# Optimization experiments

Hardware: AMD Instinct MI355X
Metric: run time of the kernel (lower is better)

## Reference

```python
import jax, jax.numpy as jnp
import numpy as np

EPS = 1e-9
LDIM = 4  # dim_g + dim_t + dim_b + dim_w


def _mvn_logpdf(v, F):
    # batched zero-mean multivariate normal log-density, v: (N,O), F: (N,O,O)
    chol = jnp.linalg.cholesky(F)
    z = jax.scipy.linalg.solve_triangular(chol, v[..., None], lower=True)[..., 0]
    quad = jnp.sum(z * z, axis=-1)
    logdet = 2.0 * jnp.sum(jnp.log(jnp.diagonal(chol, axis1=-2, axis2=-1)), axis=-1)
    k = v.shape[-1]
    return -0.5 * (quad + logdet + k * jnp.log(2.0 * jnp.pi))


def _forward(y, B_G, B_T, B_B, B_W, lambda_r1_free, lambda_r2_free,
             q_diag, r_diag, gamma1, gamma2_learnable):
    N, Nt, O = y.shape
    L = LDIM
    # ----- _build_matrices -----
    B11 = jnp.zeros((L, L)).at[0, 0].set(B_G[0, 0]).at[1, 1].set(B_T[0, 0]).at[2, 2].set(B_B[0, 0])
    B22 = jnp.zeros((L, L)).at[3, 3].set(B_W[0, 0])
    B12 = jnp.zeros((L, L)).at[3, :3].set(1.0 / 3.0)  # regime1 factors feed shared factor
    B21 = jnp.zeros((L, L))
    L1 = jnp.zeros((O, L))
    L1 = L1.at[0, 0].set(1.0).at[1, 0].set(lambda_r1_free[0]).at[2, 0].set(lambda_r1_free[1])
    L1 = L1.at[3, 1].set(1.0).at[4, 1].set(lambda_r1_free[2]).at[5, 1].set(lambda_r1_free[3])
    L1 = L1.at[6, 2].set(1.0).at[7, 2].set(lambda_r1_free[4]).at[8, 2].set(lambda_r1_free[5])
    L2 = jnp.zeros((O, L)).at[0, 3].set(1.0).at[1:, 3].set(lambda_r2_free)
    Q = jnp.diag(jnp.abs(q_diag) + 1e-4)
    R = jnp.diag(jnp.abs(r_diag) + 1e-4)
    F_JIT = 1e-5 * jnp.eye(O)
    I_L = jnp.eye(L)
    P22_CONST = 0.9999

    # ----- initial beliefs ('informative') -----
    prob0 = jnp.tile(jnp.array([0.99, 0.01], jnp.float32), (N, 1))
    eta0 = jnp.zeros((N, L), y.dtype)
    P0 = jnp.tile(jnp.diag(jnp.array([1000.0, 1000.0, 1000.0, 1e-9], y.dtype))[None], (N, 1, 1))

    def predict(B, eta, P):
        # eta: (N,L), P: (N,L,L)
        return eta @ B.T, jnp.einsum('ij,njk,lk->nil', B, P, B) + Q

    def innov(Lm, e, Pp, y_t):
        v = y_t - e @ Lm.T
        F = jnp.einsum('oi,nij,pj->nop', Lm, Pp, Lm) + R + F_JIT
        return v, F

    def kupdate(e, Pp, Lm, v, F):
        LP = jnp.einsum('oi,nij->noj', Lm, Pp)          # (N,O,L)
        K = jnp.swapaxes(jnp.linalg.solve(F, LP), -1, -2)  # P Lm^T F^{-1}, (N,L,O)
        e_u = e + jnp.einsum('nlo,no->nl', K, v)
        IKL = I_L - K @ Lm                                # (N,L,L)
        P_u = IKL @ Pp @ jnp.swapaxes(IKL, -1, -2) + jnp.einsum('nlo,op,nmp->nlm', K, R, K)
        return e_u, P_u

    def collapse(w_a, w_b, e_a, e_b, P_a, P_b):
        e = w_a[:, None] * e_a + w_b[:, None] * e_b
        da, db = e_a - e, e_b - e
        P = (w_a[:, None, None] * (P_a + da[:, :, None] * da[:, None, :])
             + w_b[:, None, None] * (P_b + db[:, :, None] * db[:, None, :]))
        return e, P

    def step(carry, y_t):
        prob, eta1, eta2, P1, P2, ll = carry
        # HMM transition: p11 depends on regime-1 state (first L-1 components)
        logit_p11 = gamma1 + eta1[:, :3] @ gamma2_learnable
        p11 = jax.nn.sigmoid(logit_p11)
        # predictions for the 4 regime transitions (origin -> destination)
        e11, Pp11 = predict(B11, eta1, P1)
        e12, Pp12 = predict(B21, eta2, P2)
        e21, Pp21 = predict(B12, eta1, P1)
        e22, Pp22 = predict(B22, eta2, P2)
        v11, F11 = innov(L1, e11, Pp11, y_t)
        v12, F12 = innov(L1, e12, Pp12, y_t)
        v21, F21 = innov(L2, e21, Pp21, y_t)
        v22, F22 = innov(L2, e22, Pp22, y_t)
        ll11 = _mvn_logpdf(v11, F11)
        ll12 = _mvn_logpdf(v12, F12)
        ll21 = _mvn_logpdf(v21, F21)
        ll22 = _mvn_logpdf(v22, F22)
        lp = jnp.log(prob + EPS)
        c11 = lp[:, 0] + jnp.log(p11 + EPS) + ll11
        c12 = lp[:, 1] + np.log(1.0 - P22_CONST + EPS) + ll12
        c21 = lp[:, 0] + jnp.log(1.0 - p11 + EPS) + ll21
        c22 = lp[:, 1] + np.log(P22_CONST + EPS) + ll22
        logp = jnp.stack([c11, c12, c21, c22], axis=1)
        ll_t = jax.scipy.special.logsumexp(logp, axis=1)
        pt = jnp.exp(logp - ll_t[:, None])
        pr1 = pt[:, 0] + pt[:, 1]
        pr2 = pt[:, 2] + pt[:, 3]
        W11 = pt[:, 0] / (pr1 + EPS)
        W12 = pt[:, 1] / (pr1 + EPS)
        W21 = pt[:, 2] / (pr2 + EPS)
        W22 = pt[:, 3] / (pr2 + EPS)
        eu11, Pu11 = kupdate(e11, Pp11, L1, v11, F11)
        eu12, Pu12 = kupdate(e12, Pp12, L1, v12, F12)
        eu21, Pu21 = kupdate(e21, Pp21, L2, v21, F21)
        eu22, Pu22 = kupdate(e22, Pp22, L2, v22, F22)
        eta1n, P1n = collapse(W11, W12, eu11, eu12, Pu11, Pu12)
        eta2n, P2n = collapse(W21, W22, eu21, eu22, Pu21, Pu22)
        probn = jnp.stack([pr1, pr2], axis=1)
        return (probn, eta1n, eta2n, P1n, P2n, ll + ll_t.sum()), None

    carry0 = (prob0, eta0, eta0, P0, P0, jnp.zeros((), y.dtype))
    (_, _, _, _, _, total_ll), _ = jax.lax.scan(step, carry0, jnp.swapaxes(y, 0, 1))
    return total_ll


def setup_inputs() -> dict:
    key = jax.random.key(0)
    ks = jax.random.split(key, 12)
    N, Nt, O = 16384, 64, 9
    f32 = jnp.float32
    return {
        'y': jax.random.normal(ks[0], (N, Nt, O), f32),
        'B_G': jax.random.uniform(ks[1], (1, 1), f32, 0.6, 0.95),  # Beta(5,1.5)-like AR coeffs
        'B_T': jax.random.uniform(ks[2], (1, 1), f32, 0.6, 0.95),
        'B_B': jax.random.uniform(ks[3], (1, 1), f32, 0.6, 0.95),
        'B_W': jax.random.uniform(ks[4], (1, 1), f32, 0.6, 0.95),
        'lambda_r1_free': jax.random.normal(ks[5], (6,), f32),
        'lambda_r2_free': jax.random.normal(ks[6], (O - 1,), f32),
        'q_diag': jax.random.uniform(ks[7], (LDIM,), f32),
        'r_diag': jax.random.uniform(ks[8], (O,), f32),
        'gamma1': jnp.abs(jax.random.normal(ks[9], (), f32)),
        'gamma2_learnable': jax.random.normal(ks[10], (LDIM - 1,), f32),
    }


def reference(y, B_G, B_T, B_B, B_W, lambda_r1_free, lambda_r2_free,
              q_diag, r_diag, gamma1, gamma2_learnable):
    return _forward(y, B_G, B_T, B_B, B_W, lambda_r1_free, lambda_r2_free,
                    q_diag, r_diag, gamma1, gamma2_learnable)
```

## Files before the change

kernel.cpp:

```cpp
#include <hip/hip_runtime.h>


typedef float v2f __attribute__((ext_vector_type(2)));

static __device__ __forceinline__ float frcp(float x)  { return __builtin_amdgcn_rcpf(x); }
static __device__ __forceinline__ float frsq(float x)  { return __builtin_amdgcn_rsqf(x); }
static __device__ __forceinline__ float fexp2(float x) { return __builtin_amdgcn_exp2f(x); }
static __device__ __forceinline__ float flog2(float x) { return __builtin_amdgcn_logf(x); }

template <int CTRL>
static __device__ __forceinline__ float dppf(float x) {
    int i = __float_as_int(x);
    i = __builtin_amdgcn_mov_dpp(i, CTRL, 0xF, 0xF, true);
    return __int_as_float(i);
}
#define ROTL 0xC9
#define ROTR 0xD2
#define XOR1 0xB1
#define XOR2 0x4E

static __device__ __forceinline__ float qsum(float x) {
    x += dppf<XOR1>(x);
    x += dppf<XOR2>(x);
    return x;
}

#define EPSF   1e-9f
#define L2E    1.4426950408889634f
#define LN2    0.6931471805599453f
#define L2_2PI_9 23.86346461225016f
#define C12F   1.00001e-4f
#define P22F   0.99990001f
#define QK     (-0.5f * L2E)

__global__ __launch_bounds__(64, 1)
void kf_kernel(const float* __restrict__ y,
               const float* __restrict__ pBG, const float* __restrict__ pBT,
               const float* __restrict__ pBB, const float* __restrict__ pBW,
               const float* __restrict__ lam1, const float* __restrict__ lam2,
               const float* __restrict__ qd,  const float* __restrict__ rd,
               const float* __restrict__ pG1, const float* __restrict__ pG2,
               float* __restrict__ partial, int N, int Nt)
{
    const int lane = threadIdx.x;
    const int j    = lane & 3;
    const int sid  = (blockIdx.x * 64 + lane) >> 2;
    const bool valid = (sid < N);
    const bool isRow = (j < 3);
    const int jj = isRow ? j : 0;
    const int rowlen = Nt * 9;
    const int nchunk = Nt / 4;

    const float bg = pBG[0], bt = pBT[0], bb = pBB[0], bw = pBW[0];
    float a[9], l2v[9], id[9], ld[9];
    a[0] = 1.f; a[1] = lam1[0]; a[2] = lam1[1];
    a[3] = 1.f; a[4] = lam1[2]; a[5] = lam1[3];
    a[6] = 1.f; a[7] = lam1[4]; a[8] = lam1[5];
    l2v[0] = 1.f;
    #pragma unroll
    for (int i = 0; i < 8; ++i) l2v[i + 1] = lam2[i];
    float l2detD = 0.f;
    #pragma unroll
    for (int o = 0; o < 9; ++o) {
        float dv = fabsf(rd[o]) + 1.0e-4f + 1.0e-5f;
        id[o] = 1.0f / dv;
        ld[o] = l2v[o] * id[o];
        l2detD += flog2(dv);
    }
    const float q0 = fabsf(qd[0]) + 1e-4f, q1 = fabsf(qd[1]) + 1e-4f;
    const float q2 = fabsf(qd[2]) + 1e-4f, q3 = fabsf(qd[3]) + 1e-4f;
    const float g0 = a[0]*a[0]*id[0] + a[1]*a[1]*id[1] + a[2]*a[2]*id[2];
    const float g1 = a[3]*a[3]*id[3] + a[4]*a[4]*id[4] + a[5]*a[5]*id[5];
    const float g2 = a[6]*a[6]*id[6] + a[7]*a[7]*id[7] + a[8]*a[8]*id[8];
    float h = 0.f;
    #pragma unroll
    for (int o = 0; o < 9; ++o) h += l2v[o] * ld[o];
    const float pk0 = q0 / (1.f + q0 * g0);
    const float pk1 = q1 / (1.f + q1 * g1);
    const float pk2 = q2 / (1.f + q2 * g2);
    const float C12D = C12F * frsq((1.f + q0*g0) * (1.f + q1*g1) * (1.f + q2*g2));
    const float gam1 = pG1[0], w0c = pG2[0], w1c = pG2[1], w2c = pG2[2];
    const float CC = -0.5f * (l2detD + L2_2PI_9);

    auto sel3 = [&](float x0, float x1, float x2) {
        float r = (jj == 1) ? x1 : x0;
        return (jj == 2) ? x2 : r;
    };
    const float aO0 = sel3(a[0], a[3], a[6]), aO1 = sel3(a[1], a[4], a[7]), aO2 = sel3(a[2], a[5], a[8]);
    const float iO0 = sel3(id[0], id[3], id[6]), iO1 = sel3(id[1], id[4], id[7]), iO2 = sel3(id[2], id[5], id[8]);
    const float lO0 = sel3(ld[0], ld[3], ld[6]), lO1 = sel3(ld[1], ld[4], ld[7]), lO2 = sel3(ld[2], ld[5], ld[8]);
    const float bS = sel3(bg, bt, bb), bN = sel3(bt, bb, bg), bP = sel3(bb, bg, bt);
    const float gS = sel3(g0, g1, g2), gN = sel3(g1, g2, g0), gP = sel3(g2, g0, g1);
    const float qS = sel3(q0, q1, q2);
    const float pkS = sel3(pk0, pk1, pk2);
    const float wS = sel3(w0c, w1c, w2c);

    auto z3 = [&](float x) { return isRow ? x : 0.0f; };

    float pf1 = 0.99f + EPSF, pf2 = 0.01f + EPSF;
    float seJ = 0.f;
    float Pr0 = 1000.f, Pr1 = 0.f, Pr2 = 0.f;
    float sm2 = 0.f, sp2 = 1e-9f;
    float acc2 = 0.0f;

    const float* row = y + (size_t)(valid ? sid : 0) * rowlen + 3 * jj;
    float A[12], B[12];
    auto loadChunk = [&](float (&buf)[12], int c) {
        const float* p = row + c * 36;
        #pragma unroll
        for (int s = 0; s < 4; ++s) {
            buf[s*3+0] = p[s*9+0];
            buf[s*3+1] = p[s*9+1];
            buf[s*3+2] = p[s*9+2];
        }
    };
    loadChunk(A, 0);

    auto step4 = [&](const float (&buf)[12]) {
        #pragma unroll
        for (int s = 0; s < 4; ++s) {
            const float y0 = buf[s*3+0], y1 = buf[s*3+1], y2 = buf[s*3+2];

            float logit = gam1 + qsum(z3(wS * seJ));
            float esig = fexp2(-logit * L2E);
            float p11 = frcp(1.f + esig);
            float pf11 = p11 + EPSF, pf21 = 1.f - p11 + EPSF;

            float epJ = bS * seJ;
            float S0 = bS*bS*Pr0 + qS;
            float S1 = bS*bN*Pr1;
            float S2 = bS*bP*Pr2;
            float M0 = S0*gS + 1.f;
            float M1 = S1*gN;
            float M2 = S2*gP;

            float v0 = y0 - aO0*epJ, v1 = y1 - aO1*epJ, v2 = y2 - aO2*epJ;
            float w0v = iO0*v0, w1v = iO1*v1, w2v = iO2*v2;
            float uJ = aO0*w0v + aO1*w1v + aO2*w2v;
            float vdv = qsum(z3(v0*w0v + v1*w1v + v2*w2v));
            float yl  = qsum(z3(lO0*y0 + lO1*y1 + lO2*y2));
            float ydy = vdv + qsum(z3(epJ * (2.f*uJ + gS*epJ)));

            float Mn0 = dppf<ROTL>(M0), Mn1 = dppf<ROTL>(M1), Mn2 = dppf<ROTL>(M2);
            float Mp0 = dppf<ROTR>(M0), Mp1 = dppf<ROTR>(M1), Mp2 = dppf<ROTR>(M2);
            float cf0 = Mn0*Mp0 - Mn1*Mp2;
            float cf1 = Mn1*Mp1 - Mn2*Mp0;
            float cf2 = Mn2*Mp2 - Mn0*Mp1;
            float det = M0*cf0 + M1*cf1 + M2*cf2;
            float rs  = frsq(det);
            float iM  = rs * rs;
            float cn0 = dppf<ROTL>(cf0), cn1 = dppf<ROTL>(cf1), cn2 = dppf<ROTL>(cf2);
            float cp0 = dppf<ROTR>(cf0), cp1 = dppf<ROTR>(cf1), cp2 = dppf<ROTR>(cf2);
            float Ci0 = iM * (S0*cf0 + S1*cn2 + S2*cp1);
            float Ci1 = iM * (S0*cf1 + S1*cn0 + S2*cp2);
            float Ci2 = iM * (S0*cf2 + S1*cn1 + S2*cp0);

            float uN = dppf<ROTL>(uJ), uP = dppf<ROTR>(uJ);
            float tJ = Ci0*uJ + Ci1*uN + Ci2*uP;
            float quad11 = vdv - qsum(z3(uJ * tJ));
            float euJ = epJ + tJ;

            float u12 = uJ + gS * epJ;
            float fJ  = pkS * u12;
            float quad12 = ydy - qsum(z3(pkS * u12 * u12));

            float seS = qsum(z3(seJ));
            float sP  = qsum(z3(Pr0 + Pr1 + Pr2));
            v2f m2v; m2v.x = seS * (1.f/3.f);       m2v.y = bw * sm2;
            v2f pvv; pvv.x = q3 + sP * (1.f/9.f);   pvv.y = bw*bw*sp2 + q3;
            v2f u1v  = (v2f){yl, yl} - m2v * (v2f){h, h};
            v2f vdav = (v2f){ydy, ydy} - m2v * ((v2f){2.f*yl, 2.f*yl} - m2v * (v2f){h, h});
            v2f denv = (v2f){1.f, 1.f} + pvv * (v2f){h, h};
            v2f rvv; rvv.x = frsq(denv.x); rvv.y = frsq(denv.y);
            v2f idev = rvv * rvv;
            v2f puv = pvv * idev;
            v2f quadv = vdav - puv * u1v * u1v;
            v2f euv = m2v + puv * u1v;

            float q11e = QK * quad11, q12e = QK * quad12;
            float q21e = QK * quadv.x, q22e = QK * quadv.y;
            float Mq = fmaxf(fmaxf(q11e, q12e), fmaxf(q21e, q22e));
            float w11 = pf1 * pf11 * rs    * fexp2(q11e - Mq);
            float w12 = pf2 * C12D         * fexp2(q12e - Mq);
            float w21 = pf1 * pf21 * rvv.x * fexp2(q21e - Mq);
            float w22 = pf2 * P22F * rvv.y * fexp2(q22e - Mq);
            float ssum = w11 + w12 + w21 + w22;
            acc2 += Mq + flog2(ssum);
            float pr1n = w11 + w12, pr2n = w21 + w22;
            float den1 = pr1n + EPSF * ssum, den2 = pr2n + EPSF * ssum;
            float inv1 = frcp(den1), inv2 = frcp(den2), issum = frcp(ssum);
            float W11 = w11*inv1, W12 = w12*inv1;
            float W21 = w21*inv2, W22 = w22*inv2;
            pf1 = pr1n * issum + EPSF;
            pf2 = pr2n * issum + EPSF;

            float neJ = W11*euJ + W12*fJ;
            float daJ = euJ - neJ, dbJ = fJ - neJ;
            float daN = dppf<ROTL>(daJ), daP = dppf<ROTR>(daJ);
            float dbN = dppf<ROTL>(dbJ), dbP = dppf<ROTR>(dbJ);
            Pr0 = W11*(Ci0 + daJ*daJ) + W12*(pkS + dbJ*dbJ);
            Pr1 = W11*(Ci1 + daJ*daN) + W12*(dbJ*dbN);
            Pr2 = W11*(Ci2 + daJ*daP) + W12*(dbJ*dbP);
            seJ = neJ;

            float nm2 = W21*euv.x + W22*euv.y;
            float dc = euv.x - nm2, dd = euv.y - nm2;
            sp2 = W21*(puv.x + dc*dc) + W22*(puv.y + dd*dd);
            sm2 = nm2;
        }
    };

    for (int c = 0; c < nchunk; c += 2) {
        if (c + 1 < nchunk) loadChunk(B, c + 1);
        step4(A);
        if (c + 2 < nchunk) loadChunk(A, c + 2);
        step4(B);
    }

    float acc = (valid && j == 0) ? (acc2 + (float)Nt * CC) * LN2 : 0.0f;
    #pragma unroll
    for (int off = 32; off; off >>= 1) acc += __shfl_down(acc, off, 64);
    if (lane == 0) partial[blockIdx.x] = acc;
}

__global__ __launch_bounds__(64)
void reduce_k(const float* __restrict__ part, float* __restrict__ out, int nb)
{
    float s = 0.f;
    for (int i = threadIdx.x; i < nb; i += 64) s += part[i];
    #pragma unroll
    for (int off = 32; off; off >>= 1) s += __shfl_down(s, off, 64);
    if (threadIdx.x == 0) out[0] = s;
}

extern "C" void kernel_launch(void* const* d_in, const int* in_sizes, int n_in,
                              void* d_out, int out_size, void* d_ws, size_t ws_size,
                              hipStream_t stream)
{
    const float* y    = (const float*)d_in[0];
    const float* pBG  = (const float*)d_in[1];
    const float* pBT  = (const float*)d_in[2];
    const float* pBB  = (const float*)d_in[3];
    const float* pBW  = (const float*)d_in[4];
    const float* lam1 = (const float*)d_in[5];
    const float* lam2 = (const float*)d_in[6];
    const float* qd   = (const float*)d_in[7];
    const float* rd   = (const float*)d_in[8];
    const float* pG1  = (const float*)d_in[9];
    const float* pG2  = (const float*)d_in[10];

    const int total = in_sizes[0];
    const int Nt = 64, O = 9;
    const int N = total / (Nt * O);
    const int blocks = (N * 4 + 63) / 64;

    float* partial = (float*)d_ws;
    kf_kernel<<<blocks, 64, 0, stream>>>(y, pBG, pBT, pBB, pBW, lam1, lam2,
                                         qd, rd, pG1, pG2, partial, N, Nt);
    reduce_k<<<1, 64, 0, stream>>>(partial, (float*)d_out, blocks);
}
```

Measured before the change: 123.8 us.

## Process two sequences per 4-lane group using packed float2 math

Each 4-lane group now filters two independent sequences at once, holding state in float2 vectors so the compiler can emit packed FP32 instructions and gain instruction-level parallelism across the serial recurrence. The launch uses half as many blocks. Row masking moves from per-use selects into constants premultiplied by a row mask. This costs roughly twice the registers per thread and halves the number of waves, which reduces latency hiding through occupancy.

Result: slower. 133.1 us (+7.5%).

```diff
diff --git a/kernel.cpp b/kernel.cpp
--- a/kernel.cpp
+++ b/kernel.cpp
@@ -19,11 +19,21 @@
 #define XOR1 0xB1
 #define XOR2 0x4E
 
-static __device__ __forceinline__ float qsum(float x) {
-    x += dppf<XOR1>(x);
-    x += dppf<XOR2>(x);
+template <int CTRL>
+static __device__ __forceinline__ v2f dpp2(v2f v) {
+    v2f r; r.x = dppf<CTRL>(v.x); r.y = dppf<CTRL>(v.y); return r;
+}
+static __device__ __forceinline__ v2f qsum2(v2f x) {
+    x += dpp2<XOR1>(x);
+    x += dpp2<XOR2>(x);
     return x;
 }
+static __device__ __forceinline__ v2f sp(float x) { return (v2f){x, x}; }
+static __device__ __forceinline__ v2f rcp2(v2f a)  { return (v2f){frcp(a.x),  frcp(a.y)};  }
+static __device__ __forceinline__ v2f rsq2(v2f a)  { return (v2f){frsq(a.x),  frsq(a.y)};  }
+static __device__ __forceinline__ v2f exp22(v2f a) { return (v2f){fexp2(a.x), fexp2(a.y)}; }
+static __device__ __forceinline__ v2f log22(v2f a) { return (v2f){flog2(a.x), flog2(a.y)}; }
+static __device__ __forceinline__ v2f max2(v2f a, v2f b) { return (v2f){fmaxf(a.x,b.x), fmaxf(a.y,b.y)}; }
 
 #define EPSF   1e-9f
 #define L2E    1.4426950408889634f
@@ -44,10 +54,12 @@
 {
     const int lane = threadIdx.x;
     const int j    = lane & 3;
-    const int sid  = (blockIdx.x * 64 + lane) >> 2;
-    const bool valid = (sid < N);
+    const int qi   = (blockIdx.x * 64 + lane) >> 2;
+    const int sidA = 2 * qi, sidB = 2 * qi + 1;
+    const bool vA = (sidA < N), vB = (sidB < N);
     const bool isRow = (j < 3);
     const int jj = isRow ? j : 0;
+    const float mrow = isRow ? 1.f : 0.f;
     const int rowlen = Nt * 9;
     const int nchunk = Nt / 4;
 
@@ -87,125 +99,141 @@
         return (jj == 2) ? x2 : r;
     };
     const float aO0 = sel3(a[0], a[3], a[6]), aO1 = sel3(a[1], a[4], a[7]), aO2 = sel3(a[2], a[5], a[8]);
-    const float iO0 = sel3(id[0], id[3], id[6]), iO1 = sel3(id[1], id[4], id[7]), iO2 = sel3(id[2], id[5], id[8]);
-    const float lO0 = sel3(ld[0], ld[3], ld[6]), lO1 = sel3(ld[1], ld[4], ld[7]), lO2 = sel3(ld[2], ld[5], ld[8]);
-    const float bS = sel3(bg, bt, bb), bN = sel3(bt, bb, bg), bP = sel3(bb, bg, bt);
+    const float iO0 = sel3(id[0], id[3], id[6]) * mrow, iO1 = sel3(id[1], id[4], id[7]) * mrow,
+                iO2 = sel3(id[2], id[5], id[8]) * mrow;
+    const float lO0 = sel3(ld[0], ld[3], ld[6]) * mrow, lO1 = sel3(ld[1], ld[4], ld[7]) * mrow,
+                lO2 = sel3(ld[2], ld[5], ld[8]) * mrow;
+    const float bS = sel3(bg, bt, bb) * mrow;
+    const float bS2 = bS * bS;
+    const float bSN = bS * sel3(bt, bb, bg);
+    const float bSP = bS * sel3(bb, bg, bt);
     const float gS = sel3(g0, g1, g2), gN = sel3(g1, g2, g0), gP = sel3(g2, g0, g1);
-    const float qS = sel3(q0, q1, q2);
-    const float pkS = sel3(pk0, pk1, pk2);
-    const float wS = sel3(w0c, w1c, w2c);
-
-    auto z3 = [&](float x) { return isRow ? x : 0.0f; };
-
-    float pf1 = 0.99f + EPSF, pf2 = 0.01f + EPSF;
-    float seJ = 0.f;
-    float Pr0 = 1000.f, Pr1 = 0.f, Pr2 = 0.f;
-    float sm2 = 0.f, sp2 = 1e-9f;
-    float acc2 = 0.0f;
-
-    const float* row = y + (size_t)(valid ? sid : 0) * rowlen + 3 * jj;
-    float A[12], B[12];
-    auto loadChunk = [&](float (&buf)[12], int c) {
-        const float* p = row + c * 36;
+    const float qS  = sel3(q0, q1, q2) * mrow;
+    const float pkS = sel3(pk0, pk1, pk2) * mrow;
+    const float wS  = sel3(w0c, w1c, w2c) * mrow;
+
+    v2f pf1 = sp(0.99f + EPSF), pf2 = sp(0.01f + EPSF);
+    v2f seJ = sp(0.f);
+    v2f Pr0 = sp(isRow ? 1000.f : 0.f), Pr1 = sp(0.f), Pr2 = sp(0.f);
+    v2f sm2 = sp(0.f), sp2 = sp(1e-9f);
+    v2f acc2 = sp(0.f);
+
+    const float* rowA = y + (size_t)(vA ? sidA : 0) * rowlen + 3 * jj;
+    const float* rowB = y + (size_t)(vB ? sidB : 0) * rowlen + 3 * jj;
+    v2f A[12], B[12];
+    auto loadChunk = [&](v2f (&buf)[12], int c) {
+        const float* pA = rowA + c * 36;
+        const float* pB = rowB + c * 36;
         #pragma unroll
         for (int s = 0; s < 4; ++s) {
-            buf[s*3+0] = p[s*9+0];
-            buf[s*3+1] = p[s*9+1];
-            buf[s*3+2] = p[s*9+2];
+            #pragma unroll
+            for (int k = 0; k < 3; ++k) {
+                buf[s*3+k].x = pA[s*9+k];
+                buf[s*3+k].y = pB[s*9+k];
+            }
         }
     };
     loadChunk(A, 0);
 
-    auto step4 = [&](const float (&buf)[12]) {
+    auto step4 = [&](const v2f (&buf)[12]) {
         #pragma unroll
         for (int s = 0; s < 4; ++s) {
-            const float y0 = buf[s*3+0], y1 = buf[s*3+1], y2 = buf[s*3+2];
-
-            float logit = gam1 + qsum(z3(wS * seJ));
-            float esig = fexp2(-logit * L2E);
-            float p11 = frcp(1.f + esig);
-            float pf11 = p11 + EPSF, pf21 = 1.f - p11 + EPSF;
-
-            float epJ = bS * seJ;
-            float S0 = bS*bS*Pr0 + qS;
-            float S1 = bS*bN*Pr1;
-            float S2 = bS*bP*Pr2;
-            float M0 = S0*gS + 1.f;
-            float M1 = S1*gN;
-            float M2 = S2*gP;
-
-            float v0 = y0 - aO0*epJ, v1 = y1 - aO1*epJ, v2 = y2 - aO2*epJ;
-            float w0v = iO0*v0, w1v = iO1*v1, w2v = iO2*v2;
-            float uJ = aO0*w0v + aO1*w1v + aO2*w2v;
-            float vdv = qsum(z3(v0*w0v + v1*w1v + v2*w2v));
-            float yl  = qsum(z3(lO0*y0 + lO1*y1 + lO2*y2));
-            float ydy = vdv + qsum(z3(epJ * (2.f*uJ + gS*epJ)));
-
-            float Mn0 = dppf<ROTL>(M0), Mn1 = dppf<ROTL>(M1), Mn2 = dppf<ROTL>(M2);
-            float Mp0 = dppf<ROTR>(M0), Mp1 = dppf<ROTR>(M1), Mp2 = dppf<ROTR>(M2);
-            float cf0 = Mn0*Mp0 - Mn1*Mp2;
-            float cf1 = Mn1*Mp1 - Mn2*Mp0;
-            float cf2 = Mn2*Mp2 - Mn0*Mp1;
-            float det = M0*cf0 + M1*cf1 + M2*cf2;
-            float rs  = frsq(det);
-            float iM  = rs * rs;
-            float cn0 = dppf<ROTL>(cf0), cn1 = dppf<ROTL>(cf1), cn2 = dppf<ROTL>(cf2);
-            float cp0 = dppf<ROTR>(cf0), cp1 = dppf<ROTR>(cf1), cp2 = dppf<ROTR>(cf2);
-            float Ci0 = iM * (S0*cf0 + S1*cn2 + S2*cp1);
-            float Ci1 = iM * (S0*cf1 + S1*cn0 + S2*cp2);
-            float Ci2 = iM * (S0*cf2 + S1*cn1 + S2*cp0);
-
-            float uN = dppf<ROTL>(uJ), uP = dppf<ROTR>(uJ);
-            float tJ = Ci0*uJ + Ci1*uN + Ci2*uP;
-            float quad11 = vdv - qsum(z3(uJ * tJ));
-            float euJ = epJ + tJ;
-
-            float u12 = uJ + gS * epJ;
-            float fJ  = pkS * u12;
-            float quad12 = ydy - qsum(z3(pkS * u12 * u12));
-
-            float seS = qsum(z3(seJ));
-            float sP  = qsum(z3(Pr0 + Pr1 + Pr2));
-            v2f m2v; m2v.x = seS * (1.f/3.f);       m2v.y = bw * sm2;
-            v2f pvv; pvv.x = q3 + sP * (1.f/9.f);   pvv.y = bw*bw*sp2 + q3;
-            v2f u1v  = (v2f){yl, yl} - m2v * (v2f){h, h};
-            v2f vdav = (v2f){ydy, ydy} - m2v * ((v2f){2.f*yl, 2.f*yl} - m2v * (v2f){h, h});
-            v2f denv = (v2f){1.f, 1.f} + pvv * (v2f){h, h};
-            v2f rvv; rvv.x = frsq(denv.x); rvv.y = frsq(denv.y);
-            v2f idev = rvv * rvv;
-            v2f puv = pvv * idev;
-            v2f quadv = vdav - puv * u1v * u1v;
-            v2f euv = m2v + puv * u1v;
-
-            float q11e = QK * quad11, q12e = QK * quad12;
-            float q21e = QK * quadv.x, q22e = QK * quadv.y;
-            float Mq = fmaxf(fmaxf(q11e, q12e), fmaxf(q21e, q22e));
-            float w11 = pf1 * pf11 * rs    * fexp2(q11e - Mq);
-            float w12 = pf2 * C12D         * fexp2(q12e - Mq);
-            float w21 = pf1 * pf21 * rvv.x * fexp2(q21e - Mq);
-            float w22 = pf2 * P22F * rvv.y * fexp2(q22e - Mq);
-            float ssum = w11 + w12 + w21 + w22;
-            acc2 += Mq + flog2(ssum);
-            float pr1n = w11 + w12, pr2n = w21 + w22;
-            float den1 = pr1n + EPSF * ssum, den2 = pr2n + EPSF * ssum;
-            float inv1 = frcp(den1), inv2 = frcp(den2), issum = frcp(ssum);
-            float W11 = w11*inv1, W12 = w12*inv1;
-            float W21 = w21*inv2, W22 = w22*inv2;
-            pf1 = pr1n * issum + EPSF;
-            pf2 = pr2n * issum + EPSF;
-
-            float neJ = W11*euJ + W12*fJ;
-            float daJ = euJ - neJ, dbJ = fJ - neJ;
-            float daN = dppf<ROTL>(daJ), daP = dppf<ROTR>(daJ);
-            float dbN = dppf<ROTL>(dbJ), dbP = dppf<ROTR>(dbJ);
-            Pr0 = W11*(Ci0 + daJ*daJ) + W12*(pkS + dbJ*dbJ);
+            const v2f y0 = buf[s*3+0], y1 = buf[s*3+1], y2 = buf[s*3+2];
+
+            v2f logit = sp(gam1) + qsum2(sp(wS) * seJ);
+            v2f esig = exp22(logit * sp(-L2E));
+            v2f p11 = rcp2(sp(1.f) + esig);
+            v2f pf11 = p11 + sp(EPSF);
+            v2f pf21 = sp(1.f) - p11 + sp(EPSF);
+
+            v2f epJ = sp(bS) * seJ;
+            v2f S0 = sp(bS2) * Pr0 + sp(qS);
+            v2f S1 = sp(bSN) * Pr1;
+            v2f S2 = sp(bSP) * Pr2;
+            v2f M0 = S0 * sp(gS) + sp(1.f);
+            v2f M1 = S1 * sp(gN);
+            v2f M2 = S2 * sp(gP);
+
+            v2f v0 = y0 - sp(aO0)*epJ;
+            v2f v1 = y1 - sp(aO1)*epJ;
+            v2f v2 = y2 - sp(aO2)*epJ;
+            v2f w0 = sp(iO0)*v0, w1 = sp(iO1)*v1, w2 = sp(iO2)*v2;
+            v2f uJ = sp(aO0)*w0 + sp(aO1)*w1 + sp(aO2)*w2;
+            v2f r1 = v0*w0 + v1*w1 + v2*w2;
+            v2f yl  = qsum2(sp(lO0)*y0 + sp(lO1)*y1 + sp(lO2)*y2);
+            v2f ydy = qsum2(r1 + epJ*(sp(2.f)*uJ + sp(gS)*epJ));
+
+            v2f Mn0 = dpp2<ROTL>(M0), Mn1 = dpp2<ROTL>(M1), Mn2 = dpp2<ROTL>(M2);
+            v2f Mp0 = dpp2<ROTR>(M0), Mp1 = dpp2<ROTR>(M1), Mp2 = dpp2<ROTR>(M2);
+            v2f cf0 = Mn0*Mp0 - Mn1*Mp2;
+            v2f cf1 = Mn1*Mp1 - Mn2*Mp0;
+            v2f cf2 = Mn2*Mp2 - Mn0*Mp1;
+            v2f det = M0*cf0 + M1*cf1 + M2*cf2;
+            v2f rs  = rsq2(det);
+            v2f iM  = rs * rs;
+            v2f cn0 = dpp2<ROTL>(cf0), cn1 = dpp2<ROTL>(cf1), cn2 = dpp2<ROTL>(cf2);
+            v2f cp0 = dpp2<ROTR>(cf0), cp1 = dpp2<ROTR>(cf1), cp2 = dpp2<ROTR>(cf2);
+            v2f Ci0 = iM * (S0*cf0 + S1*cn2 + S2*cp1);
+            v2f Ci1 = iM * (S0*cf1 + S1*cn0 + S2*cp2);
+            v2f Ci2 = iM * (S0*cf2 + S1*cn1 + S2*cp0);
+
+            v2f uN = dpp2<ROTL>(uJ), uP = dpp2<ROTR>(uJ);
+            v2f tJ = Ci0*uJ + Ci1*uN + Ci2*uP;
+            v2f quad11 = qsum2(r1 - uJ*tJ);
+            v2f euJ = epJ + tJ;
+
+            v2f u12 = uJ + sp(gS)*epJ;
+            v2f fJ  = sp(pkS) * u12;
+            v2f quad12 = ydy - qsum2(sp(pkS)*u12*u12);
+
+            v2f seS = qsum2(seJ);
+            v2f sP  = qsum2(Pr0 + Pr1 + Pr2);
+            v2f m2_1 = seS * sp(1.f/3.f);
+            v2f m2_2 = sp(bw) * sm2;
+            v2f pv_1 = sp(q3) + sP * sp(1.f/9.f);
+            v2f pv_2 = sp(bw*bw)*sp2 + sp(q3);
+            v2f u1_1 = yl - m2_1*sp(h);
+            v2f u1_2 = yl - m2_2*sp(h);
+            v2f vda_1 = ydy - m2_1*(sp(2.f)*yl - m2_1*sp(h));
+            v2f vda_2 = ydy - m2_2*(sp(2.f)*yl - m2_2*sp(h));
+            v2f den_1 = sp(1.f) + pv_1*sp(h);
+            v2f den_2 = sp(1.f) + pv_2*sp(h);
+            v2f rv_1 = rsq2(den_1), rv_2 = rsq2(den_2);
+            v2f pu_1 = pv_1*(rv_1*rv_1), pu_2 = pv_2*(rv_2*rv_2);
+            v2f quad21 = vda_1 - pu_1*u1_1*u1_1;
+            v2f quad22 = vda_2 - pu_2*u1_2*u1_2;
+            v2f eu_1 = m2_1 + pu_1*u1_1;
+            v2f eu_2 = m2_2 + pu_2*u1_2;
+
+            v2f q11e = sp(QK)*quad11, q12e = sp(QK)*quad12;
+            v2f q21e = sp(QK)*quad21, q22e = sp(QK)*quad22;
+            v2f Mq = max2(max2(q11e, q12e), max2(q21e, q22e));
+            v2f w11 = pf1*pf11*rs        * exp22(q11e - Mq);
+            v2f w12 = pf2*sp(C12D)       * exp22(q12e - Mq);
+            v2f w21 = pf1*pf21*rv_1      * exp22(q21e - Mq);
+            v2f w22 = pf2*sp(P22F)*rv_2  * exp22(q22e - Mq);
+            v2f ssum = w11 + w12 + w21 + w22;
+            acc2 += Mq + log22(ssum);
+            v2f pr1n = w11 + w12, pr2n = w21 + w22;
+            v2f den1 = pr1n + sp(EPSF)*ssum, den2 = pr2n + sp(EPSF)*ssum;
+            v2f inv1 = rcp2(den1), inv2 = rcp2(den2), issum = rcp2(ssum);
+            v2f W11 = w11*inv1, W12 = w12*inv1;
+            v2f W21 = w21*inv2, W22 = w22*inv2;
+            pf1 = pr1n*issum + sp(EPSF);
+            pf2 = pr2n*issum + sp(EPSF);
+
+            v2f neJ = W11*euJ + W12*fJ;
+            v2f daJ = euJ - neJ, dbJ = fJ - neJ;
+            v2f daN = dpp2<ROTL>(daJ), daP = dpp2<ROTR>(daJ);
+            v2f dbN = dpp2<ROTL>(dbJ), dbP = dpp2<ROTR>(dbJ);
+            Pr0 = W11*(Ci0 + daJ*daJ) + W12*(sp(pkS) + dbJ*dbJ);
             Pr1 = W11*(Ci1 + daJ*daN) + W12*(dbJ*dbN);
             Pr2 = W11*(Ci2 + daJ*daP) + W12*(dbJ*dbP);
             seJ = neJ;
 
-            float nm2 = W21*euv.x + W22*euv.y;
-            float dc = euv.x - nm2, dd = euv.y - nm2;
-            sp2 = W21*(puv.x + dc*dc) + W22*(puv.y + dd*dd);
+            v2f nm2 = W21*eu_1 + W22*eu_2;
+            v2f dc = eu_1 - nm2, dd = eu_2 - nm2;
+            sp2 = W21*(pu_1 + dc*dc) + W22*(pu_2 + dd*dd);
             sm2 = nm2;
         }
     };
@@ -217,7 +245,11 @@
         step4(B);
     }
 
-    float acc = (valid && j == 0) ? (acc2 + (float)Nt * CC) * LN2 : 0.0f;
+    float acc = 0.f;
+    if (j == 0) {
+        if (vA) acc += (acc2.x + (float)Nt * CC) * LN2;
+        if (vB) acc += (acc2.y + (float)Nt * CC) * LN2;
+    }
     #pragma unroll
     for (int off = 32; off; off >>= 1) acc += __shfl_down(acc, off, 64);
     if (lane == 0) partial[blockIdx.x] = acc;
@@ -252,7 +284,8 @@
     const int total = in_sizes[0];
     const int Nt = 64, O = 9;
     const int N = total / (Nt * O);
-    const int blocks = (N * 4 + 63) / 64;
+    const int nq = (N + 1) / 2;
+    const int blocks = (nq * 4 + 63) / 64;
 
     float* partial = (float*)d_ws;
     kf_kernel<<<blocks, 64, 0, stream>>>(y, pBG, pBT, pBB, pBW, lam1, lam2,
```

## Map one series per thread instead of four lanes with DPP exchanges

Applied to the files above, without the earlier changes.

Replaces the 4-lanes-per-series decomposition, which used DPP rotations and quad sums to share the 3x3 covariance across lanes, with one thread per series that holds the full symmetric 3x3 covariance and 9 observations in registers. This removes the cross-lane DPP traffic and the idle fourth lane, and cuts the grid to a quarter of the blocks. In exchange there is more serial arithmetic and register pressure per thread, and only 256 single-wave blocks, which may underfill the GPU's compute units and leave too few waves to hide latency.

Result: slower. 130.4 us (+5.4%).

```diff
diff --git a/kernel.cpp b/kernel.cpp
--- a/kernel.cpp
+++ b/kernel.cpp
@@ -1,29 +1,10 @@
 #include <hip/hip_runtime.h>
 
-
-typedef float v2f __attribute__((ext_vector_type(2)));
 
 static __device__ __forceinline__ float frcp(float x)  { return __builtin_amdgcn_rcpf(x); }
 static __device__ __forceinline__ float frsq(float x)  { return __builtin_amdgcn_rsqf(x); }
 static __device__ __forceinline__ float fexp2(float x) { return __builtin_amdgcn_exp2f(x); }
 static __device__ __forceinline__ float flog2(float x) { return __builtin_amdgcn_logf(x); }
-
-template <int CTRL>
-static __device__ __forceinline__ float dppf(float x) {
-    int i = __float_as_int(x);
-    i = __builtin_amdgcn_mov_dpp(i, CTRL, 0xF, 0xF, true);
-    return __int_as_float(i);
-}
-#define ROTL 0xC9
-#define ROTR 0xD2
-#define XOR1 0xB1
-#define XOR2 0x4E
-
-static __device__ __forceinline__ float qsum(float x) {
-    x += dppf<XOR1>(x);
-    x += dppf<XOR2>(x);
-    return x;
-}
 
 #define EPSF   1e-9f
 #define L2E    1.4426950408889634f
@@ -43,19 +24,15 @@
                float* __restrict__ partial, int N, int Nt)
 {
     const int lane = threadIdx.x;
-    const int j    = lane & 3;
-    const int sid  = (blockIdx.x * 64 + lane) >> 2;
+    const int sid  = blockIdx.x * 64 + lane;
     const bool valid = (sid < N);
-    const bool isRow = (j < 3);
-    const int jj = isRow ? j : 0;
     const int rowlen = Nt * 9;
-    const int nchunk = Nt / 4;
 
     const float bg = pBG[0], bt = pBT[0], bb = pBB[0], bw = pBW[0];
-    float a[9], l2v[9], id[9], ld[9];
-    a[0] = 1.f; a[1] = lam1[0]; a[2] = lam1[1];
-    a[3] = 1.f; a[4] = lam1[2]; a[5] = lam1[3];
-    a[6] = 1.f; a[7] = lam1[4]; a[8] = lam1[5];
+    const float a1 = lam1[0], a2 = lam1[1];
+    const float a4 = lam1[2], a5 = lam1[3];
+    const float a7 = lam1[4], a8 = lam1[5];
+    float l2v[9], id[9], ld[9];
     l2v[0] = 1.f;
     #pragma unroll
     for (int i = 0; i < 8; ++i) l2v[i + 1] = lam2[i];
@@ -67,11 +44,20 @@
         ld[o] = l2v[o] * id[o];
         l2detD += flog2(dv);
     }
+    const float id0 = id[0], id1 = id[1], id2 = id[2],
+                id3 = id[3], id4 = id[4], id5 = id[5],
+                id6 = id[6], id7 = id[7], id8 = id[8];
+    const float ld0 = ld[0], ld1 = ld[1], ld2 = ld[2],
+                ld3 = ld[3], ld4 = ld[4], ld5 = ld[5],
+                ld6 = ld[6], ld7 = ld[7], ld8 = ld[8];
+    const float aid0 = id0,      aid1 = a1 * id1, aid2 = a2 * id2;
+    const float aid3 = id3,      aid4 = a4 * id4, aid5 = a5 * id5;
+    const float aid6 = id6,      aid7 = a7 * id7, aid8 = a8 * id8;
     const float q0 = fabsf(qd[0]) + 1e-4f, q1 = fabsf(qd[1]) + 1e-4f;
     const float q2 = fabsf(qd[2]) + 1e-4f, q3 = fabsf(qd[3]) + 1e-4f;
-    const float g0 = a[0]*a[0]*id[0] + a[1]*a[1]*id[1] + a[2]*a[2]*id[2];
-    const float g1 = a[3]*a[3]*id[3] + a[4]*a[4]*id[4] + a[5]*a[5]*id[5];
-    const float g2 = a[6]*a[6]*id[6] + a[7]*a[7]*id[7] + a[8]*a[8]*id[8];
+    const float g0 = id0 + a1*a1*id1 + a2*a2*id2;
+    const float g1 = id3 + a4*a4*id4 + a5*a5*id5;
+    const float g2 = id6 + a7*a7*id7 + a8*a8*id8;
     float h = 0.f;
     #pragma unroll
     for (int o = 0; o < 9; ++o) h += l2v[o] * ld[o];
@@ -81,143 +67,144 @@
     const float C12D = C12F * frsq((1.f + q0*g0) * (1.f + q1*g1) * (1.f + q2*g2));
     const float gam1 = pG1[0], w0c = pG2[0], w1c = pG2[1], w2c = pG2[2];
     const float CC = -0.5f * (l2detD + L2_2PI_9);
-
-    auto sel3 = [&](float x0, float x1, float x2) {
-        float r = (jj == 1) ? x1 : x0;
-        return (jj == 2) ? x2 : r;
+    const float bg2 = bg*bg, bt2 = bt*bt, bb2 = bb*bb, bw2 = bw*bw;
+    const float bgbt = bg*bt, bgbb = bg*bb, btbb = bt*bb;
+
+    float pf1 = 0.99f + EPSF, pf2 = 0.01f + EPSF;
+    float se0 = 0.f, se1 = 0.f, se2 = 0.f;
+    float p00 = 1000.f, p01 = 0.f, p02 = 0.f, p11 = 1000.f, p12 = 0.f, p22 = 1000.f;
+    float sm2 = 0.f, sp2 = 1e-9f;
+    float acc2 = 0.f;
+
+    const float* row = y + (size_t)(valid ? sid : 0) * rowlen;
+    float A[9], B[9];
+    #pragma unroll
+    for (int k = 0; k < 9; ++k) A[k] = row[k];
+
+    auto step = [&](const float (&Y)[9]) {
+        float logit = gam1 + w0c*se0 + w1c*se1 + w2c*se2;
+        float p11s = frcp(1.f + fexp2(-logit * L2E));
+        float pf11 = p11s + EPSF, pf21 = 1.f - p11s + EPSF;
+
+        float e0 = bg*se0, e1 = bt*se1, e2 = bb*se2;
+        float s00 = bg2*p00 + q0, s11 = bt2*p11 + q1, s22 = bb2*p22 + q2;
+        float s01 = bgbt*p01, s02 = bgbb*p02, s12 = btbb*p12;
+
+        float v0 = Y[0] - e0,    v1 = Y[1] - a1*e0, v2 = Y[2] - a2*e0;
+        float v3 = Y[3] - e1,    v4 = Y[4] - a4*e1, v5 = Y[5] - a5*e1;
+        float v6 = Y[6] - e2,    v7 = Y[7] - a7*e2, v8 = Y[8] - a8*e2;
+        float u0 = aid0*v0 + aid1*v1 + aid2*v2;
+        float u1 = aid3*v3 + aid4*v4 + aid5*v5;
+        float u2 = aid6*v6 + aid7*v7 + aid8*v8;
+        float vdv = (id0*v0)*v0 + (id1*v1)*v1 + (id2*v2)*v2
+                  + (id3*v3)*v3 + (id4*v4)*v4 + (id5*v5)*v5
+                  + (id6*v6)*v6 + (id7*v7)*v7 + (id8*v8)*v8;
+        float yl  = ld0*Y[0] + ld1*Y[1] + ld2*Y[2]
+                  + ld3*Y[3] + ld4*Y[4] + ld5*Y[5]
+                  + ld6*Y[6] + ld7*Y[7] + ld8*Y[8];
+        float k0 = 2.f*u0 + g0*e0, k1 = 2.f*u1 + g1*e1, k2 = 2.f*u2 + g2*e2;
+        float ydy = vdv + e0*k0 + e1*k1 + e2*k2;
+
+        float m00 = s00*g0 + 1.f, m01 = s01*g1,       m02 = s02*g2;
+        float m10 = s01*g0,       m11 = s11*g1 + 1.f, m12 = s12*g2;
+        float m20 = s02*g0,       m21 = s12*g1,       m22 = s22*g2 + 1.f;
+        float c00 = m11*m22 - m12*m21;
+        float c01 = m12*m20 - m10*m22;
+        float c02 = m10*m21 - m11*m20;
+        float c10 = m02*m21 - m01*m22;
+        float c11 = m00*m22 - m02*m20;
+        float c12 = m01*m20 - m00*m21;
+        float c20 = m01*m12 - m02*m11;
+        float c21 = m02*m10 - m00*m12;
+        float c22 = m00*m11 - m01*m10;
+        float det = m00*c00 + m01*c01 + m02*c02;
+        float rs  = frsq(det);
+        float iM  = rs * rs;
+        float Ci00 = (s00*c00 + s01*c10 + s02*c20) * iM;
+        float Ci01 = (s00*c01 + s01*c11 + s02*c21) * iM;
+        float Ci02 = (s00*c02 + s01*c12 + s02*c22) * iM;
+        float Ci11 = (s01*c01 + s11*c11 + s12*c21) * iM;
+        float Ci12 = (s01*c02 + s11*c12 + s12*c22) * iM;
+        float Ci22 = (s02*c02 + s12*c12 + s22*c22) * iM;
+
+        float t0 = Ci00*u0 + Ci01*u1 + Ci02*u2;
+        float t1 = Ci01*u0 + Ci11*u1 + Ci12*u2;
+        float t2 = Ci02*u0 + Ci12*u1 + Ci22*u2;
+        float quad11 = vdv - (u0*t0 + u1*t1 + u2*t2);
+        float eu0 = e0 + t0, eu1 = e1 + t1, eu2 = e2 + t2;
+
+        float u120 = u0 + g0*e0, u121 = u1 + g1*e1, u122 = u2 + g2*e2;
+        float f0 = pk0*u120, f1 = pk1*u121, f2 = pk2*u122;
+        float quad12 = ydy - (f0*u120 + f1*u121 + f2*u122);
+
+        float seS = se0 + se1 + se2;
+        float sPs = p00 + p11 + p22 + 2.f*(p01 + p02 + p12);
+        float m2a = seS * (1.f/3.f);
+        float m2b = bw * sm2;
+        float pva = q3 + sPs * (1.f/9.f);
+        float pvb = bw2*sp2 + q3;
+        float u1a = yl - m2a*h;
+        float u1b = yl - m2b*h;
+        float vdaa = ydy - m2a*(2.f*yl - m2a*h);
+        float vdab = ydy - m2b*(2.f*yl - m2b*h);
+        float rva = frsq(1.f + pva*h);
+        float rvb = frsq(1.f + pvb*h);
+        float pua = pva*(rva*rva);
+        float pub = pvb*(rvb*rvb);
+        float quad21 = vdaa - pua*u1a*u1a;
+        float quad22 = vdab - pub*u1b*u1b;
+        float eua = m2a + pua*u1a;
+        float eub = m2b + pub*u1b;
+
+        float q11e = QK*quad11, q12e = QK*quad12;
+        float q21e = QK*quad21, q22e = QK*quad22;
+        float Mq = fmaxf(fmaxf(q11e, q12e), fmaxf(q21e, q22e));
+        float w11 = pf1*pf11*rs   * fexp2(q11e - Mq);
+        float w12 = pf2*C12D      * fexp2(q12e - Mq);
+        float w21 = pf1*pf21*rva  * fexp2(q21e - Mq);
+        float w22 = pf2*P22F*rvb  * fexp2(q22e - Mq);
+        float ssum = (w11 + w12) + (w21 + w22);
+        acc2 += Mq + flog2(ssum);
+        float pr1n = w11 + w12, pr2n = w21 + w22;
+        float inv1 = frcp(pr1n + EPSF*ssum);
+        float inv2 = frcp(pr2n + EPSF*ssum);
+        float issum = frcp(ssum);
+        float W11 = w11*inv1, W12 = w12*inv1;
+        float W21 = w21*inv2, W22 = w22*inv2;
+        pf1 = pr1n*issum + EPSF;
+        pf2 = pr2n*issum + EPSF;
+
+        float ne0 = W11*eu0 + W12*f0;
+        float ne1 = W11*eu1 + W12*f1;
+        float ne2 = W11*eu2 + W12*f2;
+        float da0 = eu0-ne0, da1 = eu1-ne1, da2 = eu2-ne2;
+        float db0 = f0-ne0,  db1 = f1-ne1,  db2 = f2-ne2;
+        p00 = W11*(Ci00 + da0*da0) + W12*(pk0 + db0*db0);
+        p01 = W11*(Ci01 + da0*da1) + W12*(db0*db1);
+        p02 = W11*(Ci02 + da0*da2) + W12*(db0*db2);
+        p11 = W11*(Ci11 + da1*da1) + W12*(pk1 + db1*db1);
+        p12 = W11*(Ci12 + da1*da2) + W12*(db1*db2);
+        p22 = W11*(Ci22 + da2*da2) + W12*(pk2 + db2*db2);
+        se0 = ne0; se1 = ne1; se2 = ne2;
+
+        float nm2 = W21*eua + W22*eub;
+        float dc = eua-nm2, dd = eub-nm2;
+        sp2 = W21*(pua + dc*dc) + W22*(pub + dd*dd);
+        sm2 = nm2;
     };
-    const float aO0 = sel3(a[0], a[3], a[6]), aO1 = sel3(a[1], a[4], a[7]), aO2 = sel3(a[2], a[5], a[8]);
-    const float iO0 = sel3(id[0], id[3], id[6]), iO1 = sel3(id[1], id[4], id[7]), iO2 = sel3(id[2], id[5], id[8]);
-    const float lO0 = sel3(ld[0], ld[3], ld[6]), lO1 = sel3(ld[1], ld[4], ld[7]), lO2 = sel3(ld[2], ld[5], ld[8]);
-    const float bS = sel3(bg, bt, bb), bN = sel3(bt, bb, bg), bP = sel3(bb, bg, bt);
-    const float gS = sel3(g0, g1, g2), gN = sel3(g1, g2, g0), gP = sel3(g2, g0, g1);
-    const float qS = sel3(q0, q1, q2);
-    const float pkS = sel3(pk0, pk1, pk2);
-    const float wS = sel3(w0c, w1c, w2c);
-
-    auto z3 = [&](float x) { return isRow ? x : 0.0f; };
-
-    float pf1 = 0.99f + EPSF, pf2 = 0.01f + EPSF;
-    float seJ = 0.f;
-    float Pr0 = 1000.f, Pr1 = 0.f, Pr2 = 0.f;
-    float sm2 = 0.f, sp2 = 1e-9f;
-    float acc2 = 0.0f;
-
-    const float* row = y + (size_t)(valid ? sid : 0) * rowlen + 3 * jj;
-    float A[12], B[12];
-    auto loadChunk = [&](float (&buf)[12], int c) {
-        const float* p = row + c * 36;
+
+    for (int t = 0; t < Nt; t += 2) {
         #pragma unroll
-        for (int s = 0; s < 4; ++s) {
-            buf[s*3+0] = p[s*9+0];
-            buf[s*3+1] = p[s*9+1];
-            buf[s*3+2] = p[s*9+2];
+        for (int k = 0; k < 9; ++k) B[k] = row[(t+1)*9 + k];
+        step(A);
+        if (t + 2 < Nt) {
+            #pragma unroll
+            for (int k = 0; k < 9; ++k) A[k] = row[(t+2)*9 + k];
         }
-    };
-    loadChunk(A, 0);
-
-    auto step4 = [&](const float (&buf)[12]) {
-        #pragma unroll
-        for (int s = 0; s < 4; ++s) {
-            const float y0 = buf[s*3+0], y1 = buf[s*3+1], y2 = buf[s*3+2];
-
-            float logit = gam1 + qsum(z3(wS * seJ));
-            float esig = fexp2(-logit * L2E);
-            float p11 = frcp(1.f + esig);
-            float pf11 = p11 + EPSF, pf21 = 1.f - p11 + EPSF;
-
-            float epJ = bS * seJ;
-            float S0 = bS*bS*Pr0 + qS;
-            float S1 = bS*bN*Pr1;
-            float S2 = bS*bP*Pr2;
-            float M0 = S0*gS + 1.f;
-            float M1 = S1*gN;
-            float M2 = S2*gP;
-
-            float v0 = y0 - aO0*epJ, v1 = y1 - aO1*epJ, v2 = y2 - aO2*epJ;
-            float w0v = iO0*v0, w1v = iO1*v1, w2v = iO2*v2;
-            float uJ = aO0*w0v + aO1*w1v + aO2*w2v;
-            float vdv = qsum(z3(v0*w0v + v1*w1v + v2*w2v));
-            float yl  = qsum(z3(lO0*y0 + lO1*y1 + lO2*y2));
-            float ydy = vdv + qsum(z3(epJ * (2.f*uJ + gS*epJ)));
-
-            float Mn0 = dppf<ROTL>(M0), Mn1 = dppf<ROTL>(M1), Mn2 = dppf<ROTL>(M2);
-            float Mp0 = dppf<ROTR>(M0), Mp1 = dppf<ROTR>(M1), Mp2 = dppf<ROTR>(M2);
-            float cf0 = Mn0*Mp0 - Mn1*Mp2;
-            float cf1 = Mn1*Mp1 - Mn2*Mp0;
-            float cf2 = Mn2*Mp2 - Mn0*Mp1;
-            float det = M0*cf0 + M1*cf1 + M2*cf2;
-            float rs  = frsq(det);
-            float iM  = rs * rs;
-            float cn0 = dppf<ROTL>(cf0), cn1 = dppf<ROTL>(cf1), cn2 = dppf<ROTL>(cf2);
-            float cp0 = dppf<ROTR>(cf0), cp1 = dppf<ROTR>(cf1), cp2 = dppf<ROTR>(cf2);
-            float Ci0 = iM * (S0*cf0 + S1*cn2 + S2*cp1);
-            float Ci1 = iM * (S0*cf1 + S1*cn0 + S2*cp2);
-            float Ci2 = iM * (S0*cf2 + S1*cn1 + S2*cp0);
-
-            float uN = dppf<ROTL>(uJ), uP = dppf<ROTR>(uJ);
-            float tJ = Ci0*uJ + Ci1*uN + Ci2*uP;
-            float quad11 = vdv - qsum(z3(uJ * tJ));
-            float euJ = epJ + tJ;
-
-            float u12 = uJ + gS * epJ;
-            float fJ  = pkS * u12;
-            float quad12 = ydy - qsum(z3(pkS * u12 * u12));
-
-            float seS = qsum(z3(seJ));
-            float sP  = qsum(z3(Pr0 + Pr1 + Pr2));
-            v2f m2v; m2v.x = seS * (1.f/3.f);       m2v.y = bw * sm2;
-            v2f pvv; pvv.x = q3 + sP * (1.f/9.f);   pvv.y = bw*bw*sp2 + q3;
-            v2f u1v  = (v2f){yl, yl} - m2v * (v2f){h, h};
-            v2f vdav = (v2f){ydy, ydy} - m2v * ((v2f){2.f*yl, 2.f*yl} - m2v * (v2f){h, h});
-            v2f denv = (v2f){1.f, 1.f} + pvv * (v2f){h, h};
-            v2f rvv; rvv.x = frsq(denv.x); rvv.y = frsq(denv.y);
-            v2f idev = rvv * rvv;
-            v2f puv = pvv * idev;
-            v2f quadv = vdav - puv * u1v * u1v;
-            v2f euv = m2v + puv * u1v;
-
-            float q11e = QK * quad11, q12e = QK * quad12;
-            float q21e = QK * quadv.x, q22e = QK * quadv.y;
-            float Mq = fmaxf(fmaxf(q11e, q12e), fmaxf(q21e, q22e));
-            float w11 = pf1 * pf11 * rs    * fexp2(q11e - Mq);
-            float w12 = pf2 * C12D         * fexp2(q12e - Mq);
-            float w21 = pf1 * pf21 * rvv.x * fexp2(q21e - Mq);
-            float w22 = pf2 * P22F * rvv.y * fexp2(q22e - Mq);
-            float ssum = w11 + w12 + w21 + w22;
-            acc2 += Mq + flog2(ssum);
-            float pr1n = w11 + w12, pr2n = w21 + w22;
-            float den1 = pr1n + EPSF * ssum, den2 = pr2n + EPSF * ssum;
-            float inv1 = frcp(den1), inv2 = frcp(den2), issum = frcp(ssum);
-            float W11 = w11*inv1, W12 = w12*inv1;
-            float W21 = w21*inv2, W22 = w22*inv2;
-            pf1 = pr1n * issum + EPSF;
-            pf2 = pr2n * issum + EPSF;
-
-            float neJ = W11*euJ + W12*fJ;
-            float daJ = euJ - neJ, dbJ = fJ - neJ;
-            float daN = dppf<ROTL>(daJ), daP = dppf<ROTR>(daJ);
-            float dbN = dppf<ROTL>(dbJ), dbP = dppf<ROTR>(dbJ);
-            Pr0 = W11*(Ci0 + daJ*daJ) + W12*(pkS + dbJ*dbJ);
-            Pr1 = W11*(Ci1 + daJ*daN) + W12*(dbJ*dbN);
-            Pr2 = W11*(Ci2 + daJ*daP) + W12*(dbJ*dbP);
-            seJ = neJ;
-
-            float nm2 = W21*euv.x + W22*euv.y;
-            float dc = euv.x - nm2, dd = euv.y - nm2;
-            sp2 = W21*(puv.x + dc*dc) + W22*(puv.y + dd*dd);
-            sm2 = nm2;
-        }
-    };
-
-    for (int c = 0; c < nchunk; c += 2) {
-        if (c + 1 < nchunk) loadChunk(B, c + 1);
-        step4(A);
-        if (c + 2 < nchunk) loadChunk(A, c + 2);
-        step4(B);
+        step(B);
     }
 
-    float acc = (valid && j == 0) ? (acc2 + (float)Nt * CC) * LN2 : 0.0f;
+    float acc = valid ? (acc2 + (float)Nt * CC) * LN2 : 0.f;
     #pragma unroll
     for (int off = 32; off; off >>= 1) acc += __shfl_down(acc, off, 64);
     if (lane == 0) partial[blockIdx.x] = acc;
@@ -252,7 +239,7 @@
     const int total = in_sizes[0];
     const int Nt = 64, O = 9;
     const int N = total / (Nt * O);
-    const int blocks = (N * 4 + 63) / 64;
+    const int blocks = (N + 63) / 64;
 
     float* partial = (float*)d_ws;
     kf_kernel<<<blocks, 64, 0, stream>>>(y, pBG, pBT, pBB, pBW, lam1, lam2,
```

## Precompute observation-only terms per chunk outside the recurrent filter chain

Applied to the files above, without the earlier changes.

Reformulates the innovation quantities algebraically so that terms depending only on observations (weighted projections, y'Dy, loading dot product, regime-1 shared quadratic) are computed per 4-step chunk ahead of the serial recursion. Inside the recurrence, uJ and vdv are derived from the precomputed values with fewer operations and DPP reductions, which shortens the loop-carried dependency chain. The cost is more live registers for the buffered chunk data and slightly different floating-point rounding. The second step4 call is now guarded by the chunk-count check.

Result: no change. 125.7 us (+1.5%).

```diff
diff --git a/kernel.cpp b/kernel.cpp
--- a/kernel.cpp
+++ b/kernel.cpp
@@ -116,10 +116,27 @@
     };
     loadChunk(A, 0);
 
-    auto step4 = [&](const float (&buf)[12]) {
+    struct YB4 { float uy[4], f[4], ydy[4], yl[4], q12e[4]; };
+    auto computeYB4 = [&](YB4& o, const float (&buf)[12]) {
         #pragma unroll
         for (int s = 0; s < 4; ++s) {
             const float y0 = buf[s*3+0], y1 = buf[s*3+1], y2 = buf[s*3+2];
+            float w0 = iO0*y0, w1 = iO1*y1, w2 = iO2*y2;
+            float uy = aO0*w0 + aO1*w1 + aO2*w2;
+            float ydy = qsum(z3(w0*y0 + w1*y1 + w2*y2));
+            float yl  = qsum(z3(lO0*y0 + lO1*y1 + lO2*y2));
+            float f = pkS * uy;
+            float q12 = qsum(z3(pkS * uy * uy));
+            o.uy[s] = uy; o.f[s] = f; o.ydy[s] = ydy; o.yl[s] = yl;
+            o.q12e[s] = QK * (ydy - q12);
+        }
+    };
+
+    auto step4 = [&](const YB4& yb) {
+        #pragma unroll
+        for (int s = 0; s < 4; ++s) {
+            const float uy = yb.uy[s], fJ = yb.f[s];
+            const float ydy = yb.ydy[s], yl = yb.yl[s], q12e = yb.q12e[s];
 
             float logit = gam1 + qsum(z3(wS * seJ));
             float esig = fexp2(-logit * L2E);
@@ -134,12 +151,8 @@
             float M1 = S1*gN;
             float M2 = S2*gP;
 
-            float v0 = y0 - aO0*epJ, v1 = y1 - aO1*epJ, v2 = y2 - aO2*epJ;
-            float w0v = iO0*v0, w1v = iO1*v1, w2v = iO2*v2;
-            float uJ = aO0*w0v + aO1*w1v + aO2*w2v;
-            float vdv = qsum(z3(v0*w0v + v1*w1v + v2*w2v));
-            float yl  = qsum(z3(lO0*y0 + lO1*y1 + lO2*y2));
-            float ydy = vdv + qsum(z3(epJ * (2.f*uJ + gS*epJ)));
+            float uJ = uy - gS * epJ;
+            float vdv = ydy - qsum(z3(epJ * (uy + uJ)));
 
             float Mn0 = dppf<ROTL>(M0), Mn1 = dppf<ROTL>(M1), Mn2 = dppf<ROTL>(M2);
             float Mp0 = dppf<ROTR>(M0), Mp1 = dppf<ROTR>(M1), Mp2 = dppf<ROTR>(M2);
@@ -160,10 +173,6 @@
             float quad11 = vdv - qsum(z3(uJ * tJ));
             float euJ = epJ + tJ;
 
-            float u12 = uJ + gS * epJ;
-            float fJ  = pkS * u12;
-            float quad12 = ydy - qsum(z3(pkS * u12 * u12));
-
             float seS = qsum(z3(seJ));
             float sP  = qsum(z3(Pr0 + Pr1 + Pr2));
             v2f m2v; m2v.x = seS * (1.f/3.f);       m2v.y = bw * sm2;
@@ -177,7 +186,7 @@
             v2f quadv = vdav - puv * u1v * u1v;
             v2f euv = m2v + puv * u1v;
 
-            float q11e = QK * quad11, q12e = QK * quad12;
+            float q11e = QK * quad11;
             float q21e = QK * quadv.x, q22e = QK * quadv.y;
             float Mq = fmaxf(fmaxf(q11e, q12e), fmaxf(q21e, q22e));
             float w11 = pf1 * pf11 * rs    * fexp2(q11e - Mq);
@@ -210,11 +219,15 @@
         }
     };
 
+    YB4 ya, yb;
+    computeYB4(ya, A);
     for (int c = 0; c < nchunk; c += 2) {
         if (c + 1 < nchunk) loadChunk(B, c + 1);
-        step4(A);
+        step4(ya);
+        if (c + 1 < nchunk) computeYB4(yb, B);
         if (c + 2 < nchunk) loadChunk(A, c + 2);
-        step4(B);
+        if (c + 1 < nchunk) step4(yb);
+        if (c + 2 < nchunk) computeYB4(ya, A);
     }
 
     float acc = (valid && j == 0) ? (acc2 + (float)Nt * CC) * LN2 : 0.0f;
```
